# Kernel tuning notes

Measured on AMD Instinct MI355X. Metric: run time of the kernel, lower is better.

Reference implementation:

```python
import jax, jax.numpy as jnp
import numpy as np

B, N, K, C = 8, 4096, 16, 128
HID, DEPTH = 4 * C, 2
EPS = 1e-5


def _bn(x, g, b, m, v):
    # BatchNorm1d in eval mode over the last (channel) dim
    return (x - m) * (g * jax.lax.rsqrt(v + EPS)) + b


def _ffn(x, w1, b1, w2, b2, g, bt, m, v):
    h = jax.nn.relu(jnp.einsum('bnc,ch->bnh', x, w1) + b1)
    y = jnp.einsum('bnh,hc->bnc', h, w2) + b2
    return _bn(y, g, bt, m, v)


def setup_inputs() -> dict:
    key = jax.random.key(0)
    ks = jax.random.split(key, 24)
    s = 0.05
    inp = {
        'x': jax.random.normal(ks[0], (B, N, C), jnp.float32),
        'knn_idx': jax.random.randint(ks[1], (B, N, K), 0, N, jnp.int64),
        'mlp0_w1': jax.random.normal(ks[2], (C, HID), jnp.float32) * s,
        'mlp0_b1': jax.random.normal(ks[3], (HID,), jnp.float32) * s,
        'mlp0_w2': jax.random.normal(ks[4], (HID, C), jnp.float32) * s,
        'mlp0_b2': jax.random.normal(ks[5], (C,), jnp.float32) * s,
        'mlp0_g': jax.random.uniform(ks[6], (C,), jnp.float32, 0.5, 1.5),
        'mlp0_beta': jax.random.normal(ks[7], (C,), jnp.float32) * s,
        'mlp0_m': jnp.zeros((C,), jnp.float32),
        'mlp0_v': jnp.ones((C,), jnp.float32),
        'vfr_w': jax.random.normal(ks[8], (DEPTH, C, C), jnp.float32) * s,
        'vfr_b': jax.random.normal(ks[9], (DEPTH, C), jnp.float32) * s,
        'vfr_g': jax.random.uniform(ks[10], (DEPTH, C), jnp.float32, 0.5, 1.5),
        'vfr_beta': jax.random.normal(ks[11], (DEPTH, C), jnp.float32) * s,
        'vfr_m': jnp.zeros((DEPTH, C), jnp.float32),
        'vfr_v': jnp.ones((DEPTH, C), jnp.float32),
        'ffn_w1': jax.random.normal(ks[12], (DEPTH, C, HID), jnp.float32) * s,
        'ffn_b1': jax.random.normal(ks[13], (DEPTH, HID), jnp.float32) * s,
        'ffn_w2': jax.random.normal(ks[14], (DEPTH, HID, C), jnp.float32) * s,
        'ffn_b2': jax.random.normal(ks[15], (DEPTH, C), jnp.float32) * s,
        'ffn_g': jax.random.uniform(ks[16], (DEPTH, C), jnp.float32, 0.5, 1.5),
        'ffn_beta': jax.random.normal(ks[17], (DEPTH, C), jnp.float32) * s,
        'ffn_m': jnp.zeros((DEPTH, C), jnp.float32),
        'ffn_v': jnp.ones((DEPTH, C), jnp.float32),
    }
    return inp


def reference(x, knn_idx,
              mlp0_w1, mlp0_b1, mlp0_w2, mlp0_b2, mlp0_g, mlp0_beta, mlp0_m, mlp0_v,
              vfr_w, vfr_b, vfr_g, vfr_beta, vfr_m, vfr_v,
              ffn_w1, ffn_b1, ffn_w2, ffn_b2, ffn_g, ffn_beta, ffn_m, ffn_v):
    # eval mode: DropPath is identity, BatchNorm uses running stats
    x = x + _ffn(x, mlp0_w1, mlp0_b1, mlp0_w2, mlp0_b2, mlp0_g, mlp0_beta, mlp0_m, mlp0_v)
    gather = jax.vmap(lambda pts, idx: pts[idx])  # [N,C],[N,K] -> [N,K,C]
    for i in range(DEPTH):
        # VFR: linear -> knn gather -> edge diff -> max over K -> BN
        h = jnp.einsum('bnc,cd->bnd', x, vfr_w[i]) + vfr_b[i]
        nb = gather(h, knn_idx)                      # [B,N,K,C]
        agg = jnp.max(nb - h[:, :, None, :], axis=2)  # [B,N,C]
        x = x + _bn(agg, vfr_g[i], vfr_beta[i], vfr_m[i], vfr_v[i])
        x = x + _ffn(x, ffn_w1[i], ffn_b1[i], ffn_w2[i], ffn_b2[i],
                     ffn_g[i], ffn_beta[i], ffn_m[i], ffn_v[i])
    return x
```

## Files before the change

kernel.cpp:

```cpp
#include <hip/hip_runtime.h>
#include <hip/hip_bf16.h>
#include <stdint.h>

typedef __attribute__((ext_vector_type(8))) __bf16 bf16x8;
typedef __attribute__((ext_vector_type(4))) float floatx4;

#define EPS 1e-5f

__device__ __forceinline__ unsigned short f2bf(float f) {
    union { float f; unsigned int u; } x; x.f = f;
    unsigned int r = x.u + 0x7fffu + ((x.u >> 16) & 1u);
    return (unsigned short)(r >> 16);
}

__device__ __forceinline__ float bf2f(unsigned int u) {
    union { unsigned int u; float f; } x; x.u = u << 16; return x.f;
}

struct Params {
    const float* x_in;
    const int*   knn;
    const float* w1s[3];
    const float* w2s[3];
    const float* vws[2];
    unsigned short* W1P[3];
    unsigned short* W2P[3];
    unsigned short* VTP[2];
    const float* b1s[3];
    const float* b2s[3];
    const float* gs[3];
    const float* bes[3];
    const float* ms[3];
    const float* vvs[3];
    const float* vbb[2];
    const float* vgg[2];
    const float* vbt[2];
    const float* vmm[2];
    const float* vva[2];
    float* xf;
};

__global__ __launch_bounds__(256) void pack_weights(Params P) {
    const int gtid = blockIdx.x * 256 + threadIdx.x;
    const int GT   = gridDim.x * 256;
#pragma unroll
    for (int t = 0; t < 3; ++t) {
        const float* s1 = P.w1s[t];
        unsigned short* d1 = P.W1P[t];
        for (int idx = gtid; idx < 65536; idx += GT) {
            int h = idx & 511, k = idx >> 9;
            int hf = h >> 7, w = (h >> 4) & 7, ln = h & 15;
            int ks = (k >> 5) & 3, q = (k >> 3) & 3, j = k & 7;
            d1[hf * 16384 + w * 2048 + ks * 512 + q * 128 + ln * 8 + j] = f2bf(s1[idx]);
        }
        const float* s2 = P.w2s[t];
        unsigned short* d2 = P.W2P[t];
        for (int idx = gtid; idx < 65536; idx += GT) {
            int c = idx & 127, h = idx >> 7;
            int hf = h >> 7, ks = (h >> 5) & 3, q = (h >> 3) & 3, j = h & 7;
            int w = c >> 4, ln = c & 15;
            d2[hf * 16384 + w * 2048 + ks * 512 + q * 128 + ln * 8 + j] = f2bf(s2[idx]);
        }
    }
#pragma unroll
    for (int t = 0; t < 2; ++t) {
        const float* sv = P.vws[t];
        unsigned short* dv = P.VTP[t];
        for (int idx = gtid; idx < 16384; idx += GT) {
            int c = idx & 127, k = idx >> 7;
            int ks = (k >> 5) & 3, q = (k >> 3) & 3, j = k & 7;
            int w = c >> 4, ln = c & 15;
            dv[w * 2048 + ks * 512 + q * 128 + ln * 8 + j] = f2bf(sv[idx]);
        }
    }
}

template <int LOADX, int TE, int TF, int TV>
__global__ __launch_bounds__(512, 4)
void stage(Params P, const float* __restrict__ xold_g,
           const unsigned short* __restrict__ VbIn,
           unsigned short* __restrict__ VbOut)
{
    __shared__ __align__(16) unsigned short xt[8192];
    __shared__ __align__(16) float xf32[8192];
    __shared__ __align__(16) uint2 ht2[2048];
    const int tid  = threadIdx.x;
    const int lane = tid & 63;
    const int w    = tid >> 6;
    const int q    = lane >> 4;
    const int ln   = lane & 15;
    const int sw   = ln & 7;
    const int phys = blockIdx.x;
    const int bid  = (phys & 7) * 64 + (phys >> 3);
    const int p0   = bid << 6;
    const floatx4 zero = {0.f, 0.f, 0.f, 0.f};

    if constexpr (LOADX) {
        const int r = tid >> 3, seg = tid & 7;
        const float4* src = (const float4*)(xold_g + (size_t)(p0 + r) * 128 + seg * 16);
        float4* dstf = (float4*)&xf32[r * 128 + seg * 16];
#pragma unroll
        for (int i = 0; i < 2; ++i) {
            float4 a = src[2 * i];
            float4 b = src[2 * i + 1];
            dstf[2 * i]     = a;
            dstf[2 * i + 1] = b;
            int kq = seg * 2 + i;
            uint4 pk;
            pk.x = (unsigned int)f2bf(a.x) | ((unsigned int)f2bf(a.y) << 16);
            pk.y = (unsigned int)f2bf(a.z) | ((unsigned int)f2bf(a.w) << 16);
            pk.z = (unsigned int)f2bf(b.x) | ((unsigned int)f2bf(b.y) << 16);
            pk.w = (unsigned int)f2bf(b.z) | ((unsigned int)f2bf(b.w) << 16);
            *(uint4*)&xt[(r * 16 + (kq ^ (r & 7))) * 8] = pk;
        }
    }

    if constexpr (TE >= 0) {
        const int c0 = lane << 1;
        float2 gv = *(const float2*)(P.vgg[TE] + c0);
        float2 bv = *(const float2*)(P.vbt[TE] + c0);
        float2 mv = *(const float2*)(P.vmm[TE] + c0);
        float2 vv = *(const float2*)(P.vva[TE] + c0);
        const float sc0 = gv.x * rsqrtf(vv.x + EPS);
        const float sc1 = gv.y * rsqrtf(vv.y + EPS);
#pragma unroll
        for (int it = 0; it < 8; ++it) {
            const int pl = it * 8 + w;
            const int p  = p0 + pl;
            const int b  = p >> 12;
            const size_t rowoff = (size_t)p * 128 + c0;
            unsigned int su = *(const unsigned int*)(VbIn + rowoff);
            const int4* kp4 = (const int4*)(P.knn + (size_t)p * 16);
            int4 ka = kp4[0], kb = kp4[1], kc = kp4[2], kd = kp4[3];
            const unsigned short* vbase = VbIn + (((size_t)b << 12) << 7) + c0;
            float m0 = -3.4e38f, m1 = -3.4e38f;
            unsigned int u;
#define GATH(IDX) u = *(const unsigned int*)(vbase + ((size_t)(IDX) << 7)); \
            m0 = fmaxf(m0, bf2f(u & 0xffffu)); m1 = fmaxf(m1, bf2f(u >> 16));
            GATH(ka.x) GATH(ka.y) GATH(ka.z) GATH(ka.w)
            GATH(kb.x) GATH(kb.y) GATH(kb.z) GATH(kb.w)
            GATH(kc.x) GATH(kc.y) GATH(kc.z) GATH(kc.w)
            GATH(kd.x) GATH(kd.y) GATH(kd.z) GATH(kd.w)
#undef GATH
            float s0 = bf2f(su & 0xffffu), s1 = bf2f(su >> 16);
            float y0 = (m0 - s0 - mv.x) * sc0 + bv.x;
            float y1 = (m1 - s1 - mv.y) * sc1 + bv.y;
            float2 xv = *(const float2*)(xold_g + rowoff);
            float xn0 = xv.x + y0, xn1 = xv.y + y1;
            *(float2*)&xf32[pl * 128 + c0] = make_float2(xn0, xn1);
            unsigned int pk = (unsigned int)f2bf(xn0) | ((unsigned int)f2bf(xn1) << 16);
            ((unsigned int*)xt)[(pl * 16 + ((lane >> 2) ^ (pl & 7))) * 4 + (lane & 3)] = pk;
        }
    }
    __syncthreads();

    floatx4 acc2[4];
#pragma unroll
    for (int i = 0; i < 4; ++i) acc2[i] = zero;

    const unsigned short* W1 = P.W1P[TF];
    const unsigned short* W2 = P.W2P[TF];
    const float* b1 = P.b1s[TF];

#pragma unroll
    for (int hf = 0; hf < 4; ++hf) {
        floatx4 acc1[4];
#pragma unroll
        for (int i = 0; i < 4; ++i) acc1[i] = zero;
        const unsigned short* a1 = W1 + hf * 16384 + w * 2048 + q * 128 + ln * 8;
#pragma unroll
        for (int ks = 0; ks < 4; ++ks) {
            bf16x8 af = *(const bf16x8*)(a1 + ks * 512);
#pragma unroll
            for (int nt = 0; nt < 4; ++nt) {
                bf16x8 bfr = *(const bf16x8*)&xt[((16 * nt + ln) * 16 + ((4 * ks + q) ^ sw)) * 8];
                acc1[nt] = __builtin_amdgcn_mfma_f32_16x16x32_bf16(af, bfr, acc1[nt], 0, 0, 0);
            }
        }
        {
            const int hid0 = 16 * w + 4 * q;
            const int ghid = 128 * hf + hid0;
            const float bv0 = b1[ghid + 0], bv1 = b1[ghid + 1];
            const float bv2 = b1[ghid + 2], bv3 = b1[ghid + 3];
            const int c16  = hid0 >> 3;
            const int half = q & 1;
#pragma unroll
            for (int nt = 0; nt < 4; ++nt) {
                const int pt = 16 * nt + ln;
                float v0 = acc1[nt][0] + bv0; v0 = v0 > 0.f ? v0 : 0.f;
                float v1 = acc1[nt][1] + bv1; v1 = v1 > 0.f ? v1 : 0.f;
                float v2 = acc1[nt][2] + bv2; v2 = v2 > 0.f ? v2 : 0.f;
                float v3 = acc1[nt][3] + bv3; v3 = v3 > 0.f ? v3 : 0.f;
                uint2 pk;
                pk.x = (unsigned int)f2bf(v0) | ((unsigned int)f2bf(v1) << 16);
                pk.y = (unsigned int)f2bf(v2) | ((unsigned int)f2bf(v3) << 16);
                ht2[(pt * 16 + (c16 ^ (pt & 7))) * 2 + half] = pk;
            }
        }
        __syncthreads();
        const unsigned short* b2b = W2 + hf * 16384 + w * 2048 + q * 128 + ln * 8;
#pragma unroll
        for (int ks = 0; ks < 4; ++ks) {
            bf16x8 bw = *(const bf16x8*)(b2b + ks * 512);
#pragma unroll
            for (int mt = 0; mt < 4; ++mt) {
                bf16x8 ah = *(const bf16x8*)&ht2[((16 * mt + ln) * 16 + ((4 * ks + q) ^ sw)) * 2];
                acc2[mt] = __builtin_amdgcn_mfma_f32_16x16x32_bf16(ah, bw, acc2[mt], 0, 0, 0);
            }
        }
        __syncthreads();
    }

    {
        const float* b2   = P.b2s[TF];
        const float* gam  = P.gs[TF];
        const float* bet  = P.bes[TF];
        const float* mean = P.ms[TF];
        const float* var  = P.vvs[TF];
        const int c = 16 * w + ln;
        const float bia = b2[c];
        const float sc  = gam[c] * rsqrtf(var[c] + EPS);
        const float bb  = bet[c];
        const float mu  = mean[c];
#pragma unroll
        for (int mt = 0; mt < 4; ++mt) {
#pragma unroll
            for (int r = 0; r < 4; ++r) {
                const int rl = 16 * mt + 4 * q + r;
                float v  = acc2[mt][r] + bia;
                float y  = (v - mu) * sc + bb;
                float xn = xf32[rl * 128 + c] + y;
                P.xf[(size_t)(p0 + rl) * 128 + c] = xn;
                if constexpr (TV >= 0)
                    xt[(rl * 16 + ((c >> 3) ^ (rl & 7))) * 8 + (c & 7)] = f2bf(xn);
            }
        }
    }

    if constexpr (TV >= 0) {
        __syncthreads();
        const unsigned short* VT = P.VTP[TV];
        const float* vb = P.vbb[TV];
        floatx4 acc[4];
#pragma unroll
        for (int i = 0; i < 4; ++i) acc[i] = zero;
        const unsigned short* bb2 = VT + w * 2048 + q * 128 + ln * 8;
#pragma unroll
        for (int ks = 0; ks < 4; ++ks) {
            bf16x8 bw = *(const bf16x8*)(bb2 + ks * 512);
#pragma unroll
            for (int mt = 0; mt < 4; ++mt) {
                bf16x8 ax = *(const bf16x8*)&xt[((16 * mt + ln) * 16 + ((4 * ks + q) ^ sw)) * 8];
                acc[mt] = __builtin_amdgcn_mfma_f32_16x16x32_bf16(ax, bw, acc[mt], 0, 0, 0);
            }
        }
        const int c = 16 * w + ln;
        const float bia = vb[c];
#pragma unroll
        for (int mt = 0; mt < 4; ++mt)
#pragma unroll
            for (int r = 0; r < 4; ++r)
                VbOut[(size_t)(p0 + 16 * mt + 4 * q + r) * 128 + c] = f2bf(acc[mt][r] + bia);
    }
}

extern "C" void kernel_launch(void* const* d_in, const int* in_sizes, int n_in,
                              void* d_out, int out_size, void* d_ws, size_t ws_size,
                              hipStream_t stream)
{
    Params p;
    p.x_in = (const float*)d_in[0];
    p.knn  = (const int*)d_in[1];
    const float* w1  = (const float*)d_in[2];
    const float* b1  = (const float*)d_in[3];
    const float* w2  = (const float*)d_in[4];
    const float* b2  = (const float*)d_in[5];
    const float* g0  = (const float*)d_in[6];
    const float* be0 = (const float*)d_in[7];
    const float* m0p = (const float*)d_in[8];
    const float* v0p = (const float*)d_in[9];
    const float* vw  = (const float*)d_in[10];
    const float* vbp = (const float*)d_in[11];
    const float* vgp = (const float*)d_in[12];
    const float* vbe = (const float*)d_in[13];
    const float* vmp = (const float*)d_in[14];
    const float* vvp = (const float*)d_in[15];
    const float* fw1 = (const float*)d_in[16];
    const float* fb1 = (const float*)d_in[17];
    const float* fw2 = (const float*)d_in[18];
    const float* fb2 = (const float*)d_in[19];
    const float* fg  = (const float*)d_in[20];
    const float* fbe = (const float*)d_in[21];
    const float* fm  = (const float*)d_in[22];
    const float* fv  = (const float*)d_in[23];

    p.w1s[0] = w1;  p.w1s[1] = fw1; p.w1s[2] = fw1 + 65536;
    p.w2s[0] = w2;  p.w2s[1] = fw2; p.w2s[2] = fw2 + 65536;
    p.vws[0] = vw;  p.vws[1] = vw + 16384;
    p.b1s[0] = b1;  p.b1s[1] = fb1; p.b1s[2] = fb1 + 512;
    p.b2s[0] = b2;  p.b2s[1] = fb2; p.b2s[2] = fb2 + 128;
    p.gs[0]  = g0;  p.gs[1]  = fg;  p.gs[2]  = fg + 128;
    p.bes[0] = be0; p.bes[1] = fbe; p.bes[2] = fbe + 128;
    p.ms[0]  = m0p; p.ms[1]  = fm;  p.ms[2]  = fm + 128;
    p.vvs[0] = v0p; p.vvs[1] = fv;  p.vvs[2] = fv + 128;
    p.vbb[0] = vbp; p.vbb[1] = vbp + 128;
    p.vgg[0] = vgp; p.vgg[1] = vgp + 128;
    p.vbt[0] = vbe; p.vbt[1] = vbe + 128;
    p.vmm[0] = vmp; p.vmm[1] = vmp + 128;
    p.vva[0] = vvp; p.vva[1] = vvp + 128;

    char* ws = (char*)d_ws;
    unsigned short* Vb0 = (unsigned short*)ws;
    unsigned short* Vb1 = (unsigned short*)(ws + (size_t)(8 << 20));
    unsigned short* u   = (unsigned short*)(ws + (size_t)(16 << 20));
    for (int i = 0; i < 3; ++i) p.W1P[i] = u + i * 65536;
    for (int i = 0; i < 3; ++i) p.W2P[i] = u + 196608 + i * 65536;
    for (int i = 0; i < 2; ++i) p.VTP[i] = u + 393216 + i * 16384;
    p.xf = (float*)d_out;

    pack_weights<<<dim3(512), 256, 0, stream>>>(p);
    stage<1, -1, 0, 0><<<dim3(512), 512, 0, stream>>>(p, p.x_in, nullptr, Vb0);
    stage<0,  0, 1, 1><<<dim3(512), 512, 0, stream>>>(p, p.xf, Vb0, Vb1);
    stage<0,  1, 2, -1><<<dim3(512), 512, 0, stream>>>(p, p.xf, Vb1, nullptr);
}
```

Baseline: 184.2 us.

## Retile FFN MFMA warps to 2x2 output tiles, padded LDS, drop fp32 x buffer

Reorganizes the weight packing and warp tiling so each warp computes 2x4 or 2x2 MFMA tiles, reusing loaded fragments across more MFMAs. The hidden dimension is processed in two halves of 256 instead of four of 128, which cuts barriers. The XOR-swizzled LDS layout is replaced with row padding. The fp32 copy of x in shared memory is removed and the residual is read back from the bf16 tile, which lowers LDS use but reduces residual precision. The gather now loads 8 channels per thread with 16-byte loads.

New measurement: 192.3 us. +4.4%, slower.

```diff
diff --git a/kernel.cpp b/kernel.cpp
--- a/kernel.cpp
+++ b/kernel.cpp
@@ -12,9 +12,11 @@
     unsigned int r = x.u + 0x7fffu + ((x.u >> 16) & 1u);
     return (unsigned short)(r >> 16);
 }
-
-__device__ __forceinline__ float bf2f(unsigned int u) {
+__device__ __forceinline__ float bf2f_lo(unsigned int u) {
     union { unsigned int u; float f; } x; x.u = u << 16; return x.f;
+}
+__device__ __forceinline__ float bf2f_hi(unsigned int u) {
+    union { unsigned int u; float f; } x; x.u = u & 0xffff0000u; return x.f;
 }
 
 struct Params {
@@ -49,17 +51,19 @@
         unsigned short* d1 = P.W1P[t];
         for (int idx = gtid; idx < 65536; idx += GT) {
             int h = idx & 511, k = idx >> 9;
-            int hf = h >> 7, w = (h >> 4) & 7, ln = h & 15;
+            int hf = h >> 8, w = (h >> 5) & 7, mt = (h >> 4) & 1, ln = h & 15;
             int ks = (k >> 5) & 3, q = (k >> 3) & 3, j = k & 7;
-            d1[hf * 16384 + w * 2048 + ks * 512 + q * 128 + ln * 8 + j] = f2bf(s1[idx]);
+            d1[hf * 32768 + w * 4096 + mt * 2048 + ks * 512 + q * 128 + ln * 8 + j]
+                = f2bf(s1[idx]);
         }
         const float* s2 = P.w2s[t];
         unsigned short* d2 = P.W2P[t];
         for (int idx = gtid; idx < 65536; idx += GT) {
             int c = idx & 127, h = idx >> 7;
-            int hf = h >> 7, ks = (h >> 5) & 3, q = (h >> 3) & 3, j = h & 7;
-            int w = c >> 4, ln = c & 15;
-            d2[hf * 16384 + w * 2048 + ks * 512 + q * 128 + ln * 8 + j] = f2bf(s2[idx]);
+            int hf = h >> 8, ks = (h >> 5) & 7, q = (h >> 3) & 3, j = h & 7;
+            int wg = c >> 5, nt = (c >> 4) & 1, ln = c & 15;
+            d2[hf * 32768 + wg * 8192 + nt * 4096 + ks * 512 + q * 128 + ln * 8 + j]
+                = f2bf(s2[idx]);
         }
     }
 #pragma unroll
@@ -69,8 +73,8 @@
         for (int idx = gtid; idx < 16384; idx += GT) {
             int c = idx & 127, k = idx >> 7;
             int ks = (k >> 5) & 3, q = (k >> 3) & 3, j = k & 7;
-            int w = c >> 4, ln = c & 15;
-            dv[w * 2048 + ks * 512 + q * 128 + ln * 8 + j] = f2bf(sv[idx]);
+            int wg = c >> 5, nt = (c >> 4) & 1, ln = c & 15;
+            dv[wg * 4096 + nt * 2048 + ks * 512 + q * 128 + ln * 8 + j] = f2bf(sv[idx]);
         }
     }
 }
@@ -81,134 +85,170 @@
            const unsigned short* __restrict__ VbIn,
            unsigned short* __restrict__ VbOut)
 {
-    __shared__ __align__(16) unsigned short xt[8192];
-    __shared__ __align__(16) float xf32[8192];
-    __shared__ __align__(16) uint2 ht2[2048];
+    __shared__ __align__(16) unsigned short xt[64 * 136];
+    __shared__ __align__(16) unsigned short ht[64 * 264];
     const int tid  = threadIdx.x;
     const int lane = tid & 63;
     const int w    = tid >> 6;
     const int q    = lane >> 4;
     const int ln   = lane & 15;
-    const int sw   = ln & 7;
+    const int wg   = w & 3;
+    const int wh   = w >> 2;
     const int phys = blockIdx.x;
     const int bid  = (phys & 7) * 64 + (phys >> 3);
     const int p0   = bid << 6;
     const floatx4 zero = {0.f, 0.f, 0.f, 0.f};
 
     if constexpr (LOADX) {
-        const int r = tid >> 3, seg = tid & 7;
-        const float4* src = (const float4*)(xold_g + (size_t)(p0 + r) * 128 + seg * 16);
-        float4* dstf = (float4*)&xf32[r * 128 + seg * 16];
+        const int r = tid >> 3, c = tid & 7;
+        const float4* src = (const float4*)(xold_g + (size_t)(p0 + r) * 128 + c * 16);
 #pragma unroll
         for (int i = 0; i < 2; ++i) {
-            float4 a = src[2 * i];
-            float4 b = src[2 * i + 1];
-            dstf[2 * i]     = a;
-            dstf[2 * i + 1] = b;
-            int kq = seg * 2 + i;
+            float4 a = src[2 * i], b = src[2 * i + 1];
             uint4 pk;
             pk.x = (unsigned int)f2bf(a.x) | ((unsigned int)f2bf(a.y) << 16);
             pk.y = (unsigned int)f2bf(a.z) | ((unsigned int)f2bf(a.w) << 16);
             pk.z = (unsigned int)f2bf(b.x) | ((unsigned int)f2bf(b.y) << 16);
             pk.w = (unsigned int)f2bf(b.z) | ((unsigned int)f2bf(b.w) << 16);
-            *(uint4*)&xt[(r * 16 + (kq ^ (r & 7))) * 8] = pk;
+            *(uint4*)&xt[(r * 17 + c * 2 + i) * 8] = pk;
         }
     }
 
     if constexpr (TE >= 0) {
-        const int c0 = lane << 1;
-        float2 gv = *(const float2*)(P.vgg[TE] + c0);
-        float2 bv = *(const float2*)(P.vbt[TE] + c0);
-        float2 mv = *(const float2*)(P.vmm[TE] + c0);
-        float2 vv = *(const float2*)(P.vva[TE] + c0);
-        const float sc0 = gv.x * rsqrtf(vv.x + EPS);
-        const float sc1 = gv.y * rsqrtf(vv.y + EPS);
-#pragma unroll
-        for (int it = 0; it < 8; ++it) {
-            const int pl = it * 8 + w;
+        const int ch0 = ln * 8;
+        float sc[8], of[8];
+#pragma unroll
+        for (int j2 = 0; j2 < 8; ++j2) {
+            float g  = P.vgg[TE][ch0 + j2];
+            float bt = P.vbt[TE][ch0 + j2];
+            float mu = P.vmm[TE][ch0 + j2];
+            float va = P.vva[TE][ch0 + j2];
+            sc[j2] = g * rsqrtf(va + EPS);
+            of[j2] = bt - mu * sc[j2];
+        }
+#pragma unroll
+        for (int it = 0; it < 2; ++it) {
+            const int pl = it * 32 + w * 4 + q;
             const int p  = p0 + pl;
             const int b  = p >> 12;
-            const size_t rowoff = (size_t)p * 128 + c0;
-            unsigned int su = *(const unsigned int*)(VbIn + rowoff);
-            const int4* kp4 = (const int4*)(P.knn + (size_t)p * 16);
-            int4 ka = kp4[0], kb = kp4[1], kc = kp4[2], kd = kp4[3];
-            const unsigned short* vbase = VbIn + (((size_t)b << 12) << 7) + c0;
-            float m0 = -3.4e38f, m1 = -3.4e38f;
-            unsigned int u;
-#define GATH(IDX) u = *(const unsigned int*)(vbase + ((size_t)(IDX) << 7)); \
-            m0 = fmaxf(m0, bf2f(u & 0xffffu)); m1 = fmaxf(m1, bf2f(u >> 16));
+            uint4 sv = *(const uint4*)(VbIn + (size_t)p * 128 + ch0);
+            const int* kp = P.knn + (size_t)p * 16;
+            int4 ka = *(const int4*)(kp);
+            int4 kb = *(const int4*)(kp + 4);
+            int4 kc = *(const int4*)(kp + 8);
+            int4 kd = *(const int4*)(kp + 12);
+            const unsigned short* vbase = VbIn + (((size_t)b << 12) << 7) + ch0;
+            float m[8];
+#pragma unroll
+            for (int j2 = 0; j2 < 8; ++j2) m[j2] = -3.4e38f;
+#define GATH(IDX) { uint4 u4 = *(const uint4*)(vbase + ((size_t)(IDX) << 7));      \
+            m[0] = fmaxf(m[0], bf2f_lo(u4.x)); m[1] = fmaxf(m[1], bf2f_hi(u4.x)); \
+            m[2] = fmaxf(m[2], bf2f_lo(u4.y)); m[3] = fmaxf(m[3], bf2f_hi(u4.y)); \
+            m[4] = fmaxf(m[4], bf2f_lo(u4.z)); m[5] = fmaxf(m[5], bf2f_hi(u4.z)); \
+            m[6] = fmaxf(m[6], bf2f_lo(u4.w)); m[7] = fmaxf(m[7], bf2f_hi(u4.w)); }
             GATH(ka.x) GATH(ka.y) GATH(ka.z) GATH(ka.w)
             GATH(kb.x) GATH(kb.y) GATH(kb.z) GATH(kb.w)
             GATH(kc.x) GATH(kc.y) GATH(kc.z) GATH(kc.w)
             GATH(kd.x) GATH(kd.y) GATH(kd.z) GATH(kd.w)
 #undef GATH
-            float s0 = bf2f(su & 0xffffu), s1 = bf2f(su >> 16);
-            float y0 = (m0 - s0 - mv.x) * sc0 + bv.x;
-            float y1 = (m1 - s1 - mv.y) * sc1 + bv.y;
-            float2 xv = *(const float2*)(xold_g + rowoff);
-            float xn0 = xv.x + y0, xn1 = xv.y + y1;
-            *(float2*)&xf32[pl * 128 + c0] = make_float2(xn0, xn1);
-            unsigned int pk = (unsigned int)f2bf(xn0) | ((unsigned int)f2bf(xn1) << 16);
-            ((unsigned int*)xt)[(pl * 16 + ((lane >> 2) ^ (pl & 7))) * 4 + (lane & 3)] = pk;
+            const float* xrow = xold_g + (size_t)p * 128 + ch0;
+            float4 x0 = *(const float4*)xrow;
+            float4 x1 = *(const float4*)(xrow + 4);
+            float s_[8];
+            s_[0] = bf2f_lo(sv.x); s_[1] = bf2f_hi(sv.x);
+            s_[2] = bf2f_lo(sv.y); s_[3] = bf2f_hi(sv.y);
+            s_[4] = bf2f_lo(sv.z); s_[5] = bf2f_hi(sv.z);
+            s_[6] = bf2f_lo(sv.w); s_[7] = bf2f_hi(sv.w);
+            float xo[8] = {x0.x, x0.y, x0.z, x0.w, x1.x, x1.y, x1.z, x1.w};
+            unsigned int pw[8];
+#pragma unroll
+            for (int j2 = 0; j2 < 8; ++j2) {
+                float xn = xo[j2] + (m[j2] - s_[j2]) * sc[j2] + of[j2];
+                pw[j2] = (unsigned int)f2bf(xn);
+            }
+            uint4 pk;
+            pk.x = pw[0] | (pw[1] << 16);
+            pk.y = pw[2] | (pw[3] << 16);
+            pk.z = pw[4] | (pw[5] << 16);
+            pk.w = pw[6] | (pw[7] << 16);
+            *(uint4*)&xt[(pl * 17 + ln) * 8] = pk;
         }
     }
     __syncthreads();
 
-    floatx4 acc2[4];
-#pragma unroll
-    for (int i = 0; i < 4; ++i) acc2[i] = zero;
+    floatx4 acc2[2][2];
+#pragma unroll
+    for (int i = 0; i < 2; ++i)
+#pragma unroll
+        for (int j = 0; j < 2; ++j) acc2[i][j] = zero;
 
     const unsigned short* W1 = P.W1P[TF];
     const unsigned short* W2 = P.W2P[TF];
     const float* b1 = P.b1s[TF];
 
 #pragma unroll
-    for (int hf = 0; hf < 4; ++hf) {
-        floatx4 acc1[4];
-#pragma unroll
-        for (int i = 0; i < 4; ++i) acc1[i] = zero;
-        const unsigned short* a1 = W1 + hf * 16384 + w * 2048 + q * 128 + ln * 8;
+    for (int hf = 0; hf < 2; ++hf) {
+        floatx4 acc1[2][4];
+#pragma unroll
+        for (int i = 0; i < 2; ++i)
+#pragma unroll
+            for (int j = 0; j < 4; ++j) acc1[i][j] = zero;
+        const unsigned short* a1 = W1 + hf * 32768 + w * 4096 + q * 128 + ln * 8;
 #pragma unroll
         for (int ks = 0; ks < 4; ++ks) {
-            bf16x8 af = *(const bf16x8*)(a1 + ks * 512);
-#pragma unroll
-            for (int nt = 0; nt < 4; ++nt) {
-                bf16x8 bfr = *(const bf16x8*)&xt[((16 * nt + ln) * 16 + ((4 * ks + q) ^ sw)) * 8];
-                acc1[nt] = __builtin_amdgcn_mfma_f32_16x16x32_bf16(af, bfr, acc1[nt], 0, 0, 0);
-            }
-        }
-        {
-            const int hid0 = 16 * w + 4 * q;
-            const int ghid = 128 * hf + hid0;
-            const float bv0 = b1[ghid + 0], bv1 = b1[ghid + 1];
-            const float bv2 = b1[ghid + 2], bv3 = b1[ghid + 3];
-            const int c16  = hid0 >> 3;
+            bf16x8 bfr[4];
+#pragma unroll
+            for (int nt = 0; nt < 4; ++nt)
+                bfr[nt] = *(const bf16x8*)&xt[((16 * nt + ln) * 17 + 4 * ks + q) * 8];
+#pragma unroll
+            for (int mt = 0; mt < 2; ++mt) {
+                bf16x8 af = *(const bf16x8*)(a1 + mt * 2048 + ks * 512);
+#pragma unroll
+                for (int nt = 0; nt < 4; ++nt)
+                    acc1[mt][nt] = __builtin_amdgcn_mfma_f32_16x16x32_bf16(
+                        af, bfr[nt], acc1[mt][nt], 0, 0, 0);
+            }
+        }
+        if (hf > 0) __syncthreads();
+#pragma unroll
+        for (int mt = 0; mt < 2; ++mt) {
+            const int hloc = 32 * w + 16 * mt + 4 * q;
+            const int gh   = 256 * hf + hloc;
+            const float bv0 = b1[gh], bv1 = b1[gh + 1];
+            const float bv2 = b1[gh + 2], bv3 = b1[gh + 3];
+            const int c16  = hloc >> 3;
             const int half = q & 1;
 #pragma unroll
             for (int nt = 0; nt < 4; ++nt) {
                 const int pt = 16 * nt + ln;
-                float v0 = acc1[nt][0] + bv0; v0 = v0 > 0.f ? v0 : 0.f;
-                float v1 = acc1[nt][1] + bv1; v1 = v1 > 0.f ? v1 : 0.f;
-                float v2 = acc1[nt][2] + bv2; v2 = v2 > 0.f ? v2 : 0.f;
-                float v3 = acc1[nt][3] + bv3; v3 = v3 > 0.f ? v3 : 0.f;
+                float v0 = acc1[mt][nt][0] + bv0; v0 = v0 > 0.f ? v0 : 0.f;
+                float v1 = acc1[mt][nt][1] + bv1; v1 = v1 > 0.f ? v1 : 0.f;
+                float v2 = acc1[mt][nt][2] + bv2; v2 = v2 > 0.f ? v2 : 0.f;
+                float v3 = acc1[mt][nt][3] + bv3; v3 = v3 > 0.f ? v3 : 0.f;
                 uint2 pk;
                 pk.x = (unsigned int)f2bf(v0) | ((unsigned int)f2bf(v1) << 16);
                 pk.y = (unsigned int)f2bf(v2) | ((unsigned int)f2bf(v3) << 16);
-                ht2[(pt * 16 + (c16 ^ (pt & 7))) * 2 + half] = pk;
+                *(uint2*)&ht[(pt * 33 + c16) * 8 + half * 4] = pk;
             }
         }
         __syncthreads();
-        const unsigned short* b2b = W2 + hf * 16384 + w * 2048 + q * 128 + ln * 8;
-#pragma unroll
-        for (int ks = 0; ks < 4; ++ks) {
-            bf16x8 bw = *(const bf16x8*)(b2b + ks * 512);
-#pragma unroll
-            for (int mt = 0; mt < 4; ++mt) {
-                bf16x8 ah = *(const bf16x8*)&ht2[((16 * mt + ln) * 16 + ((4 * ks + q) ^ sw)) * 2];
-                acc2[mt] = __builtin_amdgcn_mfma_f32_16x16x32_bf16(ah, bw, acc2[mt], 0, 0, 0);
-            }
-        }
-        __syncthreads();
+        const unsigned short* b2b = W2 + hf * 32768 + wg * 8192 + q * 128 + ln * 8;
+#pragma unroll
+        for (int ks = 0; ks < 8; ++ks) {
+            bf16x8 bw[2];
+#pragma unroll
+            for (int nt = 0; nt < 2; ++nt)
+                bw[nt] = *(const bf16x8*)(b2b + nt * 4096 + ks * 512);
+#pragma unroll
+            for (int mt = 0; mt < 2; ++mt) {
+                const int pt = 32 * wh + 16 * mt + ln;
+                bf16x8 ah = *(const bf16x8*)&ht[(pt * 33 + 4 * ks + q) * 8];
+#pragma unroll
+                for (int nt = 0; nt < 2; ++nt)
+                    acc2[mt][nt] = __builtin_amdgcn_mfma_f32_16x16x32_bf16(
+                        ah, bw[nt], acc2[mt][nt], 0, 0, 0);
+            }
+        }
     }
 
     {
@@ -217,22 +257,22 @@
         const float* bet  = P.bes[TF];
         const float* mean = P.ms[TF];
         const float* var  = P.vvs[TF];
-        const int c = 16 * w + ln;
-        const float bia = b2[c];
-        const float sc  = gam[c] * rsqrtf(var[c] + EPS);
-        const float bb  = bet[c];
-        const float mu  = mean[c];
-#pragma unroll
-        for (int mt = 0; mt < 4; ++mt) {
-#pragma unroll
-            for (int r = 0; r < 4; ++r) {
-                const int rl = 16 * mt + 4 * q + r;
-                float v  = acc2[mt][r] + bia;
-                float y  = (v - mu) * sc + bb;
-                float xn = xf32[rl * 128 + c] + y;
-                P.xf[(size_t)(p0 + rl) * 128 + c] = xn;
-                if constexpr (TV >= 0)
-                    xt[(rl * 16 + ((c >> 3) ^ (rl & 7))) * 8 + (c & 7)] = f2bf(xn);
+#pragma unroll
+        for (int nt = 0; nt < 2; ++nt) {
+            const int c = 32 * wg + 16 * nt + ln;
+            const float scv = gam[c] * rsqrtf(var[c] + EPS);
+            const float off = (b2[c] - mean[c]) * scv + bet[c];
+#pragma unroll
+            for (int mt = 0; mt < 2; ++mt) {
+#pragma unroll
+                for (int r = 0; r < 4; ++r) {
+                    const int pt = 32 * wh + 16 * mt + 4 * q + r;
+                    const int xa = (pt * 17 + (c >> 3)) * 8 + (c & 7);
+                    float base = bf2f_lo((unsigned int)xt[xa]);
+                    float xn = base + acc2[mt][nt][r] * scv + off;
+                    P.xf[(size_t)(p0 + pt) * 128 + c] = xn;
+                    if constexpr (TV >= 0) xt[xa] = f2bf(xn);
+                }
             }
         }
     }
@@ -240,27 +280,41 @@
     if constexpr (TV >= 0) {
         __syncthreads();
         const unsigned short* VT = P.VTP[TV];
+        floatx4 acc[2][2];
+#pragma unroll
+        for (int i = 0; i < 2; ++i)
+#pragma unroll
+            for (int j = 0; j < 2; ++j) acc[i][j] = zero;
+        const unsigned short* bb2 = VT + wg * 4096 + q * 128 + ln * 8;
+#pragma unroll
+        for (int ks = 0; ks < 4; ++ks) {
+            bf16x8 bw[2];
+#pragma unroll
+            for (int nt = 0; nt < 2; ++nt)
+                bw[nt] = *(const bf16x8*)(bb2 + nt * 2048 + ks * 512);
+#pragma unroll
+            for (int mt = 0; mt < 2; ++mt) {
+                const int pt = 32 * wh + 16 * mt + ln;
+                bf16x8 ax = *(const bf16x8*)&xt[(pt * 17 + 4 * ks + q) * 8];
+#pragma unroll
+                for (int nt = 0; nt < 2; ++nt)
+                    acc[mt][nt] = __builtin_amdgcn_mfma_f32_16x16x32_bf16(
+                        ax, bw[nt], acc[mt][nt], 0, 0, 0);
+            }
+        }
         const float* vb = P.vbb[TV];
-        floatx4 acc[4];
-#pragma unroll
-        for (int i = 0; i < 4; ++i) acc[i] = zero;
-        const unsigned short* bb2 = VT + w * 2048 + q * 128 + ln * 8;
-#pragma unroll
-        for (int ks = 0; ks < 4; ++ks) {
-            bf16x8 bw = *(const bf16x8*)(bb2 + ks * 512);
-#pragma unroll
-            for (int mt = 0; mt < 4; ++mt) {
-                bf16x8 ax = *(const bf16x8*)&xt[((16 * mt + ln) * 16 + ((4 * ks + q) ^ sw)) * 8];
-                acc[mt] = __builtin_amdgcn_mfma_f32_16x16x32_bf16(ax, bw, acc[mt], 0, 0, 0);
-            }
-        }
-        const int c = 16 * w + ln;
-        const float bia = vb[c];
-#pragma unroll
-        for (int mt = 0; mt < 4; ++mt)
-#pragma unroll
-            for (int r = 0; r < 4; ++r)
-                VbOut[(size_t)(p0 + 16 * mt + 4 * q + r) * 128 + c] = f2bf(acc[mt][r] + bia);
+#pragma unroll
+        for (int nt = 0; nt < 2; ++nt) {
+            const int c = 32 * wg + 16 * nt + ln;
+            const float bia = vb[c];
+#pragma unroll
+            for (int mt = 0; mt < 2; ++mt)
+#pragma unroll
+                for (int r = 0; r < 4; ++r) {
+                    const int pt = 32 * wh + 16 * mt + 4 * q + r;
+                    VbOut[(size_t)(p0 + pt) * 128 + c] = f2bf(acc[mt][nt][r] + bia);
+                }
+        }
     }
 }
 
```

## Fuse all stages into one persistent kernel with per-batch grid barriers

Applied to the files above, without the earlier changes.

Replaces the weight-pack kernel and three stage launches with a single kernel. Blocks synchronise through per-batch atomic spin barriers, and each batch gets its own copy of the packed weights. The activation tile stays in shared memory across stages, so the intermediate x no longer round-trips through global memory. The edge gather is widened to 16-byte loads covering 8 channels per thread. This removes launch gaps and global traffic, but relies on all 512 blocks being co-resident for the spin barriers to avoid deadlock, and duplicates the weight packing 8 times.

After: 319.9 us. 73.7% more time.

```diff
diff --git a/kernel.cpp b/kernel.cpp
--- a/kernel.cpp
+++ b/kernel.cpp
@@ -7,14 +7,16 @@
 
 #define EPS 1e-5f
 
-__device__ __forceinline__ unsigned short f2bf(float f) {
+static __device__ __forceinline__ unsigned short f2bf(float f) {
     union { float f; unsigned int u; } x; x.f = f;
     unsigned int r = x.u + 0x7fffu + ((x.u >> 16) & 1u);
     return (unsigned short)(r >> 16);
 }
-
-__device__ __forceinline__ float bf2f(unsigned int u) {
+static __device__ __forceinline__ float bf2f_lo(unsigned int u) {
     union { unsigned int u; float f; } x; x.u = u << 16; return x.f;
+}
+static __device__ __forceinline__ float bf2f_hi(unsigned int u) {
+    union { unsigned int u; float f; } x; x.u = u & 0xffff0000u; return x.f;
 }
 
 struct Params {
@@ -23,9 +25,6 @@
     const float* w1s[3];
     const float* w2s[3];
     const float* vws[2];
-    unsigned short* W1P[3];
-    unsigned short* W2P[3];
-    unsigned short* VTP[2];
     const float* b1s[3];
     const float* b2s[3];
     const float* gs[3];
@@ -37,130 +36,39 @@
     const float* vbt[2];
     const float* vmm[2];
     const float* vva[2];
+    unsigned short* wpk;
+    unsigned short* vb0;
+    unsigned short* vb1;
+    int* ctr;
     float* xf;
 };
 
-__global__ __launch_bounds__(256) void pack_weights(Params P) {
-    const int gtid = blockIdx.x * 256 + threadIdx.x;
-    const int GT   = gridDim.x * 256;
-#pragma unroll
-    for (int t = 0; t < 3; ++t) {
-        const float* s1 = P.w1s[t];
-        unsigned short* d1 = P.W1P[t];
-        for (int idx = gtid; idx < 65536; idx += GT) {
-            int h = idx & 511, k = idx >> 9;
-            int hf = h >> 7, w = (h >> 4) & 7, ln = h & 15;
-            int ks = (k >> 5) & 3, q = (k >> 3) & 3, j = k & 7;
-            d1[hf * 16384 + w * 2048 + ks * 512 + q * 128 + ln * 8 + j] = f2bf(s1[idx]);
-        }
-        const float* s2 = P.w2s[t];
-        unsigned short* d2 = P.W2P[t];
-        for (int idx = gtid; idx < 65536; idx += GT) {
-            int c = idx & 127, h = idx >> 7;
-            int hf = h >> 7, ks = (h >> 5) & 3, q = (h >> 3) & 3, j = h & 7;
-            int w = c >> 4, ln = c & 15;
-            d2[hf * 16384 + w * 2048 + ks * 512 + q * 128 + ln * 8 + j] = f2bf(s2[idx]);
-        }
-    }
-#pragma unroll
-    for (int t = 0; t < 2; ++t) {
-        const float* sv = P.vws[t];
-        unsigned short* dv = P.VTP[t];
-        for (int idx = gtid; idx < 16384; idx += GT) {
-            int c = idx & 127, k = idx >> 7;
-            int ks = (k >> 5) & 3, q = (k >> 3) & 3, j = k & 7;
-            int w = c >> 4, ln = c & 15;
-            dv[w * 2048 + ks * 512 + q * 128 + ln * 8 + j] = f2bf(sv[idx]);
-        }
-    }
-}
-
-template <int LOADX, int TE, int TF, int TV>
-__global__ __launch_bounds__(512, 4)
-void stage(Params P, const float* __restrict__ xold_g,
-           const unsigned short* __restrict__ VbIn,
-           unsigned short* __restrict__ VbOut)
+static __device__ __forceinline__ void bbar(int* c) {
+    __syncthreads();
+    if (threadIdx.x == 0) {
+        __hip_atomic_fetch_add(c, 1, __ATOMIC_RELEASE, __HIP_MEMORY_SCOPE_AGENT);
+        int spins = 0;
+        while (__hip_atomic_load(c, __ATOMIC_ACQUIRE, __HIP_MEMORY_SCOPE_AGENT) < 64
+               && spins < (1 << 26)) {
+            ++spins;
+            __builtin_amdgcn_s_sleep(2);
+        }
+    }
+    __syncthreads();
+}
+
+static __device__ __forceinline__ void ffn_block(
+    const Params& P, const unsigned short* WPK, int t, bool last,
+    unsigned short* xt, float* xf32, uint2* ht2,
+    int p0, int w, int q, int ln, int sw)
 {
-    __shared__ __align__(16) unsigned short xt[8192];
-    __shared__ __align__(16) float xf32[8192];
-    __shared__ __align__(16) uint2 ht2[2048];
-    const int tid  = threadIdx.x;
-    const int lane = tid & 63;
-    const int w    = tid >> 6;
-    const int q    = lane >> 4;
-    const int ln   = lane & 15;
-    const int sw   = ln & 7;
-    const int phys = blockIdx.x;
-    const int bid  = (phys & 7) * 64 + (phys >> 3);
-    const int p0   = bid << 6;
     const floatx4 zero = {0.f, 0.f, 0.f, 0.f};
-
-    if constexpr (LOADX) {
-        const int r = tid >> 3, seg = tid & 7;
-        const float4* src = (const float4*)(xold_g + (size_t)(p0 + r) * 128 + seg * 16);
-        float4* dstf = (float4*)&xf32[r * 128 + seg * 16];
-#pragma unroll
-        for (int i = 0; i < 2; ++i) {
-            float4 a = src[2 * i];
-            float4 b = src[2 * i + 1];
-            dstf[2 * i]     = a;
-            dstf[2 * i + 1] = b;
-            int kq = seg * 2 + i;
-            uint4 pk;
-            pk.x = (unsigned int)f2bf(a.x) | ((unsigned int)f2bf(a.y) << 16);
-            pk.y = (unsigned int)f2bf(a.z) | ((unsigned int)f2bf(a.w) << 16);
-            pk.z = (unsigned int)f2bf(b.x) | ((unsigned int)f2bf(b.y) << 16);
-            pk.w = (unsigned int)f2bf(b.z) | ((unsigned int)f2bf(b.w) << 16);
-            *(uint4*)&xt[(r * 16 + (kq ^ (r & 7))) * 8] = pk;
-        }
-    }
-
-    if constexpr (TE >= 0) {
-        const int c0 = lane << 1;
-        float2 gv = *(const float2*)(P.vgg[TE] + c0);
-        float2 bv = *(const float2*)(P.vbt[TE] + c0);
-        float2 mv = *(const float2*)(P.vmm[TE] + c0);
-        float2 vv = *(const float2*)(P.vva[TE] + c0);
-        const float sc0 = gv.x * rsqrtf(vv.x + EPS);
-        const float sc1 = gv.y * rsqrtf(vv.y + EPS);
-#pragma unroll
-        for (int it = 0; it < 8; ++it) {
-            const int pl = it * 8 + w;
-            const int p  = p0 + pl;
-            const int b  = p >> 12;
-            const size_t rowoff = (size_t)p * 128 + c0;
-            unsigned int su = *(const unsigned int*)(VbIn + rowoff);
-            const int4* kp4 = (const int4*)(P.knn + (size_t)p * 16);
-            int4 ka = kp4[0], kb = kp4[1], kc = kp4[2], kd = kp4[3];
-            const unsigned short* vbase = VbIn + (((size_t)b << 12) << 7) + c0;
-            float m0 = -3.4e38f, m1 = -3.4e38f;
-            unsigned int u;
-#define GATH(IDX) u = *(const unsigned int*)(vbase + ((size_t)(IDX) << 7)); \
-            m0 = fmaxf(m0, bf2f(u & 0xffffu)); m1 = fmaxf(m1, bf2f(u >> 16));
-            GATH(ka.x) GATH(ka.y) GATH(ka.z) GATH(ka.w)
-            GATH(kb.x) GATH(kb.y) GATH(kb.z) GATH(kb.w)
-            GATH(kc.x) GATH(kc.y) GATH(kc.z) GATH(kc.w)
-            GATH(kd.x) GATH(kd.y) GATH(kd.z) GATH(kd.w)
-#undef GATH
-            float s0 = bf2f(su & 0xffffu), s1 = bf2f(su >> 16);
-            float y0 = (m0 - s0 - mv.x) * sc0 + bv.x;
-            float y1 = (m1 - s1 - mv.y) * sc1 + bv.y;
-            float2 xv = *(const float2*)(xold_g + rowoff);
-            float xn0 = xv.x + y0, xn1 = xv.y + y1;
-            *(float2*)&xf32[pl * 128 + c0] = make_float2(xn0, xn1);
-            unsigned int pk = (unsigned int)f2bf(xn0) | ((unsigned int)f2bf(xn1) << 16);
-            ((unsigned int*)xt)[(pl * 16 + ((lane >> 2) ^ (pl & 7))) * 4 + (lane & 3)] = pk;
-        }
-    }
-    __syncthreads();
-
     floatx4 acc2[4];
 #pragma unroll
     for (int i = 0; i < 4; ++i) acc2[i] = zero;
-
-    const unsigned short* W1 = P.W1P[TF];
-    const unsigned short* W2 = P.W2P[TF];
-    const float* b1 = P.b1s[TF];
+    const unsigned short* W1 = WPK + t * 65536;
+    const unsigned short* W2 = WPK + 196608 + t * 65536;
+    const float* b1 = P.b1s[t];
 
 #pragma unroll
     for (int hf = 0; hf < 4; ++hf) {
@@ -179,9 +87,9 @@
         }
         {
             const int hid0 = 16 * w + 4 * q;
-            const int ghid = 128 * hf + hid0;
-            const float bv0 = b1[ghid + 0], bv1 = b1[ghid + 1];
-            const float bv2 = b1[ghid + 2], bv3 = b1[ghid + 3];
+            const int gh   = 128 * hf + hid0;
+            const float bv0 = b1[gh], bv1 = b1[gh + 1];
+            const float bv2 = b1[gh + 2], bv3 = b1[gh + 3];
             const int c16  = hid0 >> 3;
             const int half = q & 1;
 #pragma unroll
@@ -210,58 +118,216 @@
         }
         __syncthreads();
     }
-
     {
-        const float* b2   = P.b2s[TF];
-        const float* gam  = P.gs[TF];
-        const float* bet  = P.bes[TF];
-        const float* mean = P.ms[TF];
-        const float* var  = P.vvs[TF];
+        const float* b2   = P.b2s[t];
+        const float* gam  = P.gs[t];
+        const float* bet  = P.bes[t];
+        const float* mean = P.ms[t];
+        const float* var  = P.vvs[t];
         const int c = 16 * w + ln;
-        const float bia = b2[c];
-        const float sc  = gam[c] * rsqrtf(var[c] + EPS);
-        const float bb  = bet[c];
-        const float mu  = mean[c];
+        const float scv = gam[c] * rsqrtf(var[c] + EPS);
+        const float off = (b2[c] - mean[c]) * scv + bet[c];
 #pragma unroll
         for (int mt = 0; mt < 4; ++mt) {
 #pragma unroll
             for (int r = 0; r < 4; ++r) {
                 const int rl = 16 * mt + 4 * q + r;
-                float v  = acc2[mt][r] + bia;
-                float y  = (v - mu) * sc + bb;
-                float xn = xf32[rl * 128 + c] + y;
-                P.xf[(size_t)(p0 + rl) * 128 + c] = xn;
-                if constexpr (TV >= 0)
+                float xn = xf32[rl * 128 + c] + acc2[mt][r] * scv + off;
+                if (last) {
+                    P.xf[(size_t)(p0 + rl) * 128 + c] = xn;
+                } else {
+                    xf32[rl * 128 + c] = xn;
                     xt[(rl * 16 + ((c >> 3) ^ (rl & 7))) * 8 + (c & 7)] = f2bf(xn);
-            }
-        }
-    }
-
-    if constexpr (TV >= 0) {
-        __syncthreads();
-        const unsigned short* VT = P.VTP[TV];
-        const float* vb = P.vbb[TV];
-        floatx4 acc[4];
-#pragma unroll
-        for (int i = 0; i < 4; ++i) acc[i] = zero;
-        const unsigned short* bb2 = VT + w * 2048 + q * 128 + ln * 8;
-#pragma unroll
-        for (int ks = 0; ks < 4; ++ks) {
-            bf16x8 bw = *(const bf16x8*)(bb2 + ks * 512);
-#pragma unroll
-            for (int mt = 0; mt < 4; ++mt) {
-                bf16x8 ax = *(const bf16x8*)&xt[((16 * mt + ln) * 16 + ((4 * ks + q) ^ sw)) * 8];
-                acc[mt] = __builtin_amdgcn_mfma_f32_16x16x32_bf16(ax, bw, acc[mt], 0, 0, 0);
-            }
-        }
-        const int c = 16 * w + ln;
-        const float bia = vb[c];
-#pragma unroll
-        for (int mt = 0; mt < 4; ++mt)
-#pragma unroll
-            for (int r = 0; r < 4; ++r)
-                VbOut[(size_t)(p0 + 16 * mt + 4 * q + r) * 128 + c] = f2bf(acc[mt][r] + bia);
-    }
+                }
+            }
+        }
+    }
+}
+
+static __device__ __forceinline__ void vfr_block(
+    const Params& P, const unsigned short* WPK, int tv,
+    unsigned short* xt, unsigned short* VbOut,
+    int p0, int w, int q, int ln, int sw)
+{
+    __syncthreads();
+    const floatx4 zero = {0.f, 0.f, 0.f, 0.f};
+    const unsigned short* VT = WPK + 393216 + tv * 16384;
+    floatx4 acc[4];
+#pragma unroll
+    for (int i = 0; i < 4; ++i) acc[i] = zero;
+    const unsigned short* bb2 = VT + w * 2048 + q * 128 + ln * 8;
+#pragma unroll
+    for (int ks = 0; ks < 4; ++ks) {
+        bf16x8 bw = *(const bf16x8*)(bb2 + ks * 512);
+#pragma unroll
+        for (int mt = 0; mt < 4; ++mt) {
+            bf16x8 ax = *(const bf16x8*)&xt[((16 * mt + ln) * 16 + ((4 * ks + q) ^ sw)) * 8];
+            acc[mt] = __builtin_amdgcn_mfma_f32_16x16x32_bf16(ax, bw, acc[mt], 0, 0, 0);
+        }
+    }
+    const int c = 16 * w + ln;
+    const float bia = P.vbb[tv][c];
+#pragma unroll
+    for (int mt = 0; mt < 4; ++mt)
+#pragma unroll
+        for (int r = 0; r < 4; ++r) {
+            const int pt = 16 * mt + 4 * q + r;
+            VbOut[(size_t)(p0 + pt) * 128 + c] = f2bf(acc[mt][r] + bia);
+        }
+}
+
+static __device__ __forceinline__ void edge_block(
+    const Params& P, int te, const unsigned short* VbIn,
+    unsigned short* xt, float* xf32,
+    int p0, int batch, int w, int q, int ln)
+{
+    const int ch0 = ln * 8;
+    float4 ga = *(const float4*)(P.vgg[te] + ch0), gb = *(const float4*)(P.vgg[te] + ch0 + 4);
+    float4 ba = *(const float4*)(P.vbt[te] + ch0), bb = *(const float4*)(P.vbt[te] + ch0 + 4);
+    float4 ma = *(const float4*)(P.vmm[te] + ch0), mb = *(const float4*)(P.vmm[te] + ch0 + 4);
+    float4 va = *(const float4*)(P.vva[te] + ch0), vb = *(const float4*)(P.vva[te] + ch0 + 4);
+    float sc[8], of[8];
+    const float gv[8] = {ga.x, ga.y, ga.z, ga.w, gb.x, gb.y, gb.z, gb.w};
+    const float bv[8] = {ba.x, ba.y, ba.z, ba.w, bb.x, bb.y, bb.z, bb.w};
+    const float mv[8] = {ma.x, ma.y, ma.z, ma.w, mb.x, mb.y, mb.z, mb.w};
+    const float vv[8] = {va.x, va.y, va.z, va.w, vb.x, vb.y, vb.z, vb.w};
+#pragma unroll
+    for (int j = 0; j < 8; ++j) {
+        sc[j] = gv[j] * rsqrtf(vv[j] + EPS);
+        of[j] = bv[j] - mv[j] * sc[j];
+    }
+#pragma unroll
+    for (int it = 0; it < 2; ++it) {
+        const int pl = it * 32 + w * 4 + q;
+        const int p  = p0 + pl;
+        uint4 sv = *(const uint4*)(VbIn + (size_t)p * 128 + ch0);
+        const int* kp = P.knn + (size_t)p * 16;
+        int4 ka = *(const int4*)(kp);
+        int4 kb = *(const int4*)(kp + 4);
+        int4 kc = *(const int4*)(kp + 8);
+        int4 kd = *(const int4*)(kp + 12);
+        const unsigned short* vbase = VbIn + ((size_t)batch << 19) + ch0;
+        float m[8];
+#pragma unroll
+        for (int j = 0; j < 8; ++j) m[j] = -3.4e38f;
+#define GATH(IDX) { uint4 u4 = *(const uint4*)(vbase + ((size_t)(IDX) << 7));      \
+        m[0] = fmaxf(m[0], bf2f_lo(u4.x)); m[1] = fmaxf(m[1], bf2f_hi(u4.x)); \
+        m[2] = fmaxf(m[2], bf2f_lo(u4.y)); m[3] = fmaxf(m[3], bf2f_hi(u4.y)); \
+        m[4] = fmaxf(m[4], bf2f_lo(u4.z)); m[5] = fmaxf(m[5], bf2f_hi(u4.z)); \
+        m[6] = fmaxf(m[6], bf2f_lo(u4.w)); m[7] = fmaxf(m[7], bf2f_hi(u4.w)); }
+        GATH(ka.x) GATH(ka.y) GATH(ka.z) GATH(ka.w)
+        GATH(kb.x) GATH(kb.y) GATH(kb.z) GATH(kb.w)
+        GATH(kc.x) GATH(kc.y) GATH(kc.z) GATH(kc.w)
+        GATH(kd.x) GATH(kd.y) GATH(kd.z) GATH(kd.w)
+#undef GATH
+        float s_[8];
+        s_[0] = bf2f_lo(sv.x); s_[1] = bf2f_hi(sv.x);
+        s_[2] = bf2f_lo(sv.y); s_[3] = bf2f_hi(sv.y);
+        s_[4] = bf2f_lo(sv.z); s_[5] = bf2f_hi(sv.z);
+        s_[6] = bf2f_lo(sv.w); s_[7] = bf2f_hi(sv.w);
+        float* xr = &xf32[pl * 128 + ch0];
+        float4 x0 = *(const float4*)xr;
+        float4 x1 = *(const float4*)(xr + 4);
+        float xo[8] = {x0.x, x0.y, x0.z, x0.w, x1.x, x1.y, x1.z, x1.w};
+        float xn[8];
+        unsigned int pw[8];
+#pragma unroll
+        for (int j = 0; j < 8; ++j) {
+            xn[j] = xo[j] + (m[j] - s_[j]) * sc[j] + of[j];
+            pw[j] = (unsigned int)f2bf(xn[j]);
+        }
+        *(float4*)xr       = make_float4(xn[0], xn[1], xn[2], xn[3]);
+        *(float4*)(xr + 4) = make_float4(xn[4], xn[5], xn[6], xn[7]);
+        uint4 pk;
+        pk.x = pw[0] | (pw[1] << 16);
+        pk.y = pw[2] | (pw[3] << 16);
+        pk.z = pw[4] | (pw[5] << 16);
+        pk.w = pw[6] | (pw[7] << 16);
+        *(uint4*)&xt[(pl * 16 + (ln ^ (pl & 7))) * 8] = pk;
+    }
+}
+
+__global__ __launch_bounds__(512, 4) void fused(Params P) {
+    __shared__ __align__(16) unsigned short xt[8192];
+    __shared__ __align__(16) float xf32[8192];
+    __shared__ __align__(16) uint2 ht2[2048];
+    const int tid   = threadIdx.x;
+    const int lane  = tid & 63;
+    const int w     = tid >> 6;
+    const int q     = lane >> 4;
+    const int ln    = lane & 15;
+    const int sw    = ln & 7;
+    const int phys  = blockIdx.x;
+    const int batch = phys & 7;
+    const int blk   = phys >> 3;
+    const int p0    = batch * 4096 + blk * 64;
+    unsigned short* WPK = P.wpk + (size_t)batch * 425984;
+
+    {
+        const int bt = blk * 512 + tid;
+#pragma unroll
+        for (int t = 0; t < 3; ++t) {
+            const float* s1 = P.w1s[t];
+            unsigned short* d1 = WPK + t * 65536;
+            for (int idx = bt; idx < 65536; idx += 32768) {
+                int h = idx & 511, k = idx >> 9;
+                int hf = h >> 7, ww = (h >> 4) & 7, l2 = h & 15;
+                int ks = (k >> 5) & 3, qq = (k >> 3) & 3, j = k & 7;
+                d1[hf * 16384 + ww * 2048 + ks * 512 + qq * 128 + l2 * 8 + j] = f2bf(s1[idx]);
+            }
+            const float* s2 = P.w2s[t];
+            unsigned short* d2 = WPK + 196608 + t * 65536;
+            for (int idx = bt; idx < 65536; idx += 32768) {
+                int c = idx & 127, h = idx >> 7;
+                int hf = h >> 7, ks = (h >> 5) & 3, qq = (h >> 3) & 3, j = h & 7;
+                int ww = c >> 4, l2 = c & 15;
+                d2[hf * 16384 + ww * 2048 + ks * 512 + qq * 128 + l2 * 8 + j] = f2bf(s2[idx]);
+            }
+        }
+#pragma unroll
+        for (int t = 0; t < 2; ++t) {
+            const float* svv = P.vws[t];
+            unsigned short* dv = WPK + 393216 + t * 16384;
+            for (int idx = bt; idx < 16384; idx += 32768) {
+                int c = idx & 127, k = idx >> 7;
+                int ks = (k >> 5) & 3, qq = (k >> 3) & 3, j = k & 7;
+                int ww = c >> 4, l2 = c & 15;
+                dv[ww * 2048 + ks * 512 + qq * 128 + l2 * 8 + j] = f2bf(svv[idx]);
+            }
+        }
+    }
+
+    {
+        const int r = tid >> 3, cc = tid & 7;
+        const float4* src = (const float4*)(P.x_in + (size_t)(p0 + r) * 128 + cc * 16);
+        float4* dstf = (float4*)&xf32[r * 128 + cc * 16];
+#pragma unroll
+        for (int i = 0; i < 2; ++i) {
+            float4 a = src[2 * i], b = src[2 * i + 1];
+            dstf[2 * i]     = a;
+            dstf[2 * i + 1] = b;
+            int kq = cc * 2 + i;
+            uint4 pk;
+            pk.x = (unsigned int)f2bf(a.x) | ((unsigned int)f2bf(a.y) << 16);
+            pk.y = (unsigned int)f2bf(a.z) | ((unsigned int)f2bf(a.w) << 16);
+            pk.z = (unsigned int)f2bf(b.x) | ((unsigned int)f2bf(b.y) << 16);
+            pk.w = (unsigned int)f2bf(b.z) | ((unsigned int)f2bf(b.w) << 16);
+            *(uint4*)&xt[(r * 16 + (kq ^ (r & 7))) * 8] = pk;
+        }
+    }
+
+    bbar(P.ctr + batch * 16);
+    ffn_block(P, WPK, 0, false, xt, xf32, ht2, p0, w, q, ln, sw);
+    vfr_block(P, WPK, 0, xt, P.vb0, p0, w, q, ln, sw);
+    bbar(P.ctr + (8 + batch) * 16);
+    edge_block(P, 0, P.vb0, xt, xf32, p0, batch, w, q, ln);
+    __syncthreads();
+    ffn_block(P, WPK, 1, false, xt, xf32, ht2, p0, w, q, ln, sw);
+    vfr_block(P, WPK, 1, xt, P.vb1, p0, w, q, ln, sw);
+    bbar(P.ctr + (16 + batch) * 16);
+    edge_block(P, 1, P.vb1, xt, xf32, p0, batch, w, q, ln);
+    __syncthreads();
+    ffn_block(P, WPK, 2, true, xt, xf32, ht2, p0, w, q, ln, sw);
 }
 
 extern "C" void kernel_launch(void* const* d_in, const int* in_sizes, int n_in,
@@ -310,16 +376,12 @@
     p.vva[0] = vvp; p.vva[1] = vvp + 128;
 
     char* ws = (char*)d_ws;
-    unsigned short* Vb0 = (unsigned short*)ws;
-    unsigned short* Vb1 = (unsigned short*)(ws + (size_t)(8 << 20));
-    unsigned short* u   = (unsigned short*)(ws + (size_t)(16 << 20));
-    for (int i = 0; i < 3; ++i) p.W1P[i] = u + i * 65536;
-    for (int i = 0; i < 3; ++i) p.W2P[i] = u + 196608 + i * 65536;
-    for (int i = 0; i < 2; ++i) p.VTP[i] = u + 393216 + i * 16384;
-    p.xf = (float*)d_out;
-
-    pack_weights<<<dim3(512), 256, 0, stream>>>(p);
-    stage<1, -1, 0, 0><<<dim3(512), 512, 0, stream>>>(p, p.x_in, nullptr, Vb0);
-    stage<0,  0, 1, 1><<<dim3(512), 512, 0, stream>>>(p, p.xf, Vb0, Vb1);
-    stage<0,  1, 2, -1><<<dim3(512), 512, 0, stream>>>(p, p.xf, Vb1, nullptr);
-}
+    p.vb0 = (unsigned short*)ws;
+    p.vb1 = (unsigned short*)(ws + (size_t)(8 << 20));
+    p.wpk = (unsigned short*)(ws + (size_t)(16 << 20));
+    p.ctr = (int*)(ws + (size_t)(24 << 20));
+    p.xf  = (float*)d_out;
+
+    hipMemsetAsync(p.ctr, 0, 3 * 8 * 16 * sizeof(int), stream);
+    fused<<<dim3(512), dim3(512), 0, stream>>>(p);
+}
```
